# Optimization experiments

Hardware: AMD Instinct MI355X
Metric: run time of the kernel (lower is better)

Reference implementation:

```python
import jax, jax.numpy as jnp
import numpy as np

N_USERS = 20000
N_ITEMS = 20000
H0, H1, H2 = 256, 512, 256  # hidden = [256, 512, 256]
B = 4096
LN_EPS = 1e-5


def _ln(x, g, b):
    m = jnp.mean(x, axis=-1, keepdims=True)
    v = jnp.mean(jnp.square(x - m), axis=-1, keepdims=True)
    return (x - m) * jax.lax.rsqrt(v + LN_EPS) * g + b


def setup_inputs() -> dict:
    key = jax.random.key(0)
    ks = jax.random.split(key, 12)
    s = 0.02
    inp = {
        "user_idx": jax.random.randint(ks[0], (B,), 0, N_USERS),
        "item_idx": jax.random.randint(ks[1], (B,), 0, N_ITEMS),
        # (n_users+1, n_items+1) binary interaction matrix, stored as bool
        "interactions": jax.random.bernoulli(ks[2], 0.05, (N_USERS + 1, N_ITEMS + 1)),
        # proj_u / proj_i (bias=False), torch Linear layout (out, in)
        "Wu": jax.random.normal(ks[3], (H0, N_ITEMS), jnp.float32) * s,
        "Wi": jax.random.normal(ks[4], (H0, N_USERS), jnp.float32) * s,
        # rep_u: Linear(H0,H1)+LN+ReLU, Linear(H1,H2)+LN+ReLU (dropout=eval identity)
        "W1": jax.random.normal(ks[5], (H1, H0), jnp.float32) * s,
        "b1": jnp.zeros((H1,), jnp.float32),
        "g1": jnp.ones((H1,), jnp.float32),
        "be1": jnp.zeros((H1,), jnp.float32),
        "W2": jax.random.normal(ks[6], (H2, H1), jnp.float32) * s,
        "b2": jnp.zeros((H2,), jnp.float32),
        "g2": jnp.ones((H2,), jnp.float32),
        "be2": jnp.zeros((H2,), jnp.float32),
        # logit layer
        "Wl": jax.random.normal(ks[7], (1, H2), jnp.float32) * s,
        "bl": jnp.zeros((1,), jnp.float32),
    }
    return inp


def reference(user_idx, item_idx, interactions, Wu, Wi, W1, b1, g1, be1,
              W2, b2, g2, be2, Wl, bl):
    b_arange = jnp.arange(user_idx.shape[0])

    # --- user history embedding: gather row, zero target item, project, MLP ---
    u_slice = interactions[user_idx, :-1].astype(jnp.float32)      # (B, n_items)
    u_slice = u_slice.at[b_arange, item_idx].set(0.0)
    u = u_slice @ Wu.T                                             # (B, H0)
    u = jax.nn.relu(_ln(u @ W1.T + b1, g1, be1))                   # (B, H1)
    user_rep = jax.nn.relu(_ln(u @ W2.T + b2, g2, be2))            # (B, H2)

    # --- item history embedding: gather column, zero target user, project ---
    i_slice = interactions.T[item_idx][:, :-1].astype(jnp.float32)  # (B, n_users)
    i_slice = i_slice.at[b_arange, user_idx].set(0.0)
    item_rep = i_slice @ Wi.T                                      # (B, H0); rep_i is an empty Sequential in source

    pred_vector = user_rep * item_rep                              # (B, H2) == (B, H0)
    logit = (pred_vector @ Wl.T + bl).squeeze(-1)                  # (B,)
    return logit
```

## Files before the change

### kernel.cpp

```cpp
#include <hip/hip_runtime.h>

#define N_USERS 20000
#define N_ITEMS 20000
#define NI1     20001
#define HB      4096
#define H0      256
#define H1      512
#define H2      256
#define PKW     632
#define PKB     (PKW*4)
#define NWF     12501251

typedef unsigned short u16;
typedef unsigned char  u8;
typedef unsigned int   u32;
typedef unsigned long long u64;

typedef __attribute__((ext_vector_type(8))) __bf16 bf16x8;
typedef __attribute__((ext_vector_type(4))) float  f32x4;

__device__ __forceinline__ u16 f2bf(float f) {
  u32 u = __float_as_uint(f);
  u32 r = (u + 0x7FFFu + ((u >> 16) & 1u)) >> 16;
  return (u16)r;
}

__global__ __launch_bounds__(256) void k_detect(const u8* __restrict__ inter,
                                                int* __restrict__ flag) {
  __shared__ u32 cnt[4];
  if (threadIdx.x < 4) cnt[threadIdx.x] = 0;
  __syncthreads();
  u32 loc0 = 0, loc1 = 0, loc2 = 0, loc3 = 0;
  for (int i = threadIdx.x; i < 16384; i += 256) {
    u32 w = ((const u32*)inter)[i];
    loc0 += (w & 0x000000FFu) ? 1u : 0u;
    loc1 += (w & 0x0000FF00u) ? 1u : 0u;
    loc2 += (w & 0x00FF0000u) ? 1u : 0u;
    loc3 += (w & 0xFF000000u) ? 1u : 0u;
  }
  atomicAdd(&cnt[0], loc0); atomicAdd(&cnt[1], loc1);
  atomicAdd(&cnt[2], loc2); atomicAdd(&cnt[3], loc3);
  __syncthreads();
  if (threadIdx.x == 0) {
    int lay;
    if (cnt[1] != 0)      lay = 0;
    else if (cnt[0] != 0) lay = 1;
    else                  lay = 2;
    *flag = lay;
  }
}

__global__ __launch_bounds__(256) void k_packF(const u8* __restrict__ inter,
                                               u32* __restrict__ pkF,
                                               const int* __restrict__ flag) {
  int lay = *flag;
  __shared__ u32 nibs[4][8][64];
  const size_t TE = (size_t)NI1 * NI1;
  const int NG = (int)((TE + 8191) / 8192);
  int wave = threadIdx.x >> 6, lane = threadIdx.x & 63;
  const u32* base32 = (const u32*)inter;
  for (int g = blockIdx.x; g < NG; g += gridDim.x) {
    size_t E0 = (size_t)g * 8192 + (size_t)wave * 2048;
    bool full = ((size_t)(g + 1) * 8192) <= TE;
    if (lay != 0) {
      if (full) {
        #pragma unroll
        for (int t = 0; t < 8; ++t) {
          size_t e = E0 + (size_t)t * 256 + lane * 4;
          uint4 v = *(const uint4*)(base32 + e);
          nibs[wave][t][lane] = (v.x ? 1u : 0u) | (v.y ? 2u : 0u) |
                                (v.z ? 4u : 0u) | (v.w ? 8u : 0u);
        }
      } else {
        #pragma unroll
        for (int t = 0; t < 8; ++t) {
          size_t e = E0 + (size_t)t * 256 + lane * 4;
          u32 n = 0;
          #pragma unroll
          for (int c = 0; c < 4; ++c)
            if (e + c < TE && base32[e + c]) n |= 1u << c;
          nibs[wave][t][lane] = n;
        }
      }
    } else {
      #pragma unroll
      for (int t = 0; t < 8; ++t) {
        size_t e = E0 + (size_t)t * 256 + lane * 4;
        u32 n = 0;
        #pragma unroll
        for (int c = 0; c < 4; ++c)
          if (e + c < TE && inter[e + c]) n |= 1u << c;
        nibs[wave][t][lane] = n;
      }
    }
    __syncthreads();
    {
      int t = lane >> 3, j = lane & 7;
      u32 wrd = 0;
      #pragma unroll
      for (int k = 0; k < 8; ++k) wrd |= nibs[wave][t][8 * j + k] << (4 * k);
      size_t wg = (size_t)g * 256 + wave * 64 + lane;
      if (wg < NWF) pkF[wg] = wrd;
    }
    __syncthreads();
  }
}

__global__ __launch_bounds__(256) void k_realign(const u32* __restrict__ pkF,
                                                 u32* __restrict__ pk) {
  int r = blockIdx.x;
  int base = 625 * r + (r >> 5);
  int s = r & 31;
  for (int w = threadIdx.x; w < PKW; w += 256) {
    u32 val = 0;
    if (w < 625) {
      u32 lo = pkF[base + w];
      u32 hi = pkF[base + w + 1];
      val = s ? ((lo >> s) | (hi << (32 - s))) : lo;
    }
    pk[(size_t)r * PKW + w] = val;
  }
}

#define HDSTEP(J, M)                                      \
  _Pragma("unroll")                                       \
  for (int k = 0; k < 32; ++k) if (!(k & J)) {            \
    u32 tt = (a[k] ^ (a[k | J] >> J)) & M;                \
    a[k] ^= tt; a[k | J] ^= tt << J;                      \
  }

__global__ __launch_bounds__(256) void k_bitT(const u32* __restrict__ pk,
                                              u32* __restrict__ pkT) {
  __shared__ u32 in_l[512][17];
  __shared__ u32 out_l[32][16][17];
  int t = threadIdx.x;
  int vt = blockIdx.x % 40, wt = blockIdx.x / 40;
  int v0 = vt * 16, wc0 = wt * 16;
  int lw = t & 15, lr = t >> 4;
  for (int ch = 0; ch < 32; ++ch) {
    int rloc = ch * 16 + lr;
    int R = v0 * 32 + rloc;
    int W = wc0 + lw;
    u32 val = 0;
    if (R < N_USERS && W < PKW) val = pk[(size_t)R * PKW + W];
    in_l[rloc][lw] = val;
  }
  __syncthreads();
  u32 a[32];
  #pragma unroll
  for (int j = 0; j < 32; ++j) a[j] = in_l[lr * 32 + j][lw];
  HDSTEP(16, 0x0000FFFFu)
  HDSTEP(8,  0x00FF00FFu)
  HDSTEP(4,  0x0F0F0F0Fu)
  HDSTEP(2,  0x33333333u)
  HDSTEP(1,  0x55555555u)
  #pragma unroll
  for (int i = 0; i < 32; ++i) out_l[i][lw][lr] = __brev(a[31 - i]);
  __syncthreads();
  for (int ch = 0; ch < 32; ++ch) {
    int rloc = ch * 16 + lr;
    int C = wc0 * 32 + rloc;
    int V = v0 + lw;
    if (C < N_ITEMS && V < PKW)
      pkT[(size_t)C * PKW + V] = out_l[rloc & 31][rloc >> 5][lw];
  }
}

__global__ __launch_bounds__(256) void k_convert2(const float* __restrict__ Wu,
                                                  const float* __restrict__ Wi,
                                                  u16* __restrict__ Wub,
                                                  u16* __restrict__ Wib) {
  const int n4 = H0 * N_ITEMS / 4;
  int stride = gridDim.x * 256;
  for (int i = blockIdx.x * 256 + threadIdx.x; i < 2 * n4; i += stride) {
    const float* in = (i < n4) ? Wu : Wi;
    u16* out = (i < n4) ? Wub : Wib;
    int idx = (i < n4) ? i : i - n4;
    float4 v = ((const float4*)in)[idx];
    u64 p = (u64)f2bf(v.x) | ((u64)f2bf(v.y) << 16) |
            ((u64)f2bf(v.z) << 32) | ((u64)f2bf(v.w) << 48);
    ((u64*)out)[idx] = p;
  }
}

__global__ __launch_bounds__(256) void k_transpose2(const float* __restrict__ W1,
                                                    float* __restrict__ W1T,
                                                    const float* __restrict__ W2,
                                                    float* __restrict__ W2T) {
  __shared__ float tile[32][33];
  int bid = blockIdx.x;
  const float* in; float* out; int R, C, b;
  if (bid < 128) { in = W1; out = W1T; R = H1; C = H0; b = bid; }
  else           { in = W2; out = W2T; R = H2; C = H1; b = bid - 128; }
  int nbx = C >> 5;
  int bx = b % nbx, by = b / nbx;
  int c0 = bx * 32, r0 = by * 32;
  int lx = threadIdx.x & 31, ly = threadIdx.x >> 5;
  #pragma unroll
  for (int j = 0; j < 4; ++j)
    tile[ly + 8*j][lx] = in[(size_t)(r0 + ly + 8*j) * C + c0 + lx];
  __syncthreads();
  #pragma unroll
  for (int j = 0; j < 4; ++j)
    out[(size_t)(c0 + ly + 8*j) * R + r0 + lx] = tile[lx][ly + 8*j];
}

__global__ __launch_bounds__(1024) void k_sort(const int* __restrict__ item_idx,
                                               int* __restrict__ perm) {
  __shared__ u32 cnt[N_ITEMS];
  __shared__ u32 tsum[1024];
  int t = threadIdx.x;
  for (int i = t; i < N_ITEMS; i += 1024) cnt[i] = 0;
  __syncthreads();
  for (int b = t; b < HB; b += 1024) atomicAdd(&cnt[item_idx[b]], 1u);
  __syncthreads();
  u32 s = 0;
  int base = t * 20;
  for (int j = 0; j < 20; ++j) { int i = base + j; if (i < N_ITEMS) s += cnt[i]; }
  tsum[t] = s;
  __syncthreads();
  for (int off = 1; off < 1024; off <<= 1) {
    u32 v = (t >= off) ? tsum[t - off] : 0u;
    __syncthreads();
    tsum[t] += v;
    __syncthreads();
  }
  u32 run = tsum[t] - s;
  for (int j = 0; j < 20; ++j) {
    int i = base + j;
    if (i < N_ITEMS) { u32 c = cnt[i]; cnt[i] = run; run += c; }
  }
  __syncthreads();
  for (int b = t; b < HB; b += 1024) {
    int v = item_idx[b];
    u32 pos = atomicAdd(&cnt[v], 1u);
    perm[pos] = b;
  }
}

__global__ __launch_bounds__(256, 4) void k_gemm(
    const u32* __restrict__ pk, const u32* __restrict__ pkT,
    const int* __restrict__ user_idx, const int* __restrict__ item_idx,
    const int* __restrict__ perm,
    const u16* __restrict__ Wub, const u16* __restrict__ Wib,
    float* __restrict__ u0, float* __restrict__ u0b,
    float* __restrict__ ir, float* __restrict__ irb) {
  __shared__ __attribute__((aligned(16))) u16 Bls[2][32 * 256];
  __shared__ __attribute__((aligned(16))) uint2 lut8[16];
  __shared__ u32 pbase[128];
  __shared__ int prow[128];

  int bid = blockIdx.x;
  int kh = bid >> 9;
  int mode_item = (bid >> 8) & 1;
  int lid = bid & 255;
  int M0 = (lid >> 3) * 128;
  int N0 = (lid & 7) * 32;
  int tid = threadIdx.x;
  const u16* Wb = mode_item ? Wib : Wub;
  const u8* Pk = (const u8*)(mode_item ? pkT : pk);
  float* Cout = mode_item ? (kh ? irb : ir) : (kh ? u0b : u0);

  if (tid < 16) {
    u32 v = tid;
    lut8[tid].x = ((v & 1u) ? 0x3F80u : 0u) | ((v & 2u) ? 0x3F800000u : 0u);
    lut8[tid].y = ((v & 4u) ? 0x3F80u : 0u) | ((v & 8u) ? 0x3F800000u : 0u);
  }
  if (tid < 128) {
    int s = M0 + tid;
    if (mode_item) { int p = perm[s]; prow[tid] = p; pbase[tid] = (u32)item_idx[p] * PKB; }
    else           { prow[tid] = s;   pbase[tid] = (u32)user_idx[s] * PKB; }
  }
  __syncthreads();

  f32x4 acc[2][2];
  #pragma unroll
  for (int a = 0; a < 2; ++a)
    #pragma unroll
    for (int b = 0; b < 2; ++b)
      #pragma unroll
      for (int j = 0; j < 4; ++j) acc[a][b][j] = 0.f;

  int lane = tid & 63, wave = tid >> 6;
  int WM = wave * 32;
  int lrow = lane & 15;
  int lk8 = lane >> 4;
  int sh = lk8 * 8;

  u32 pb0 = pbase[WM + lrow];
  u32 pb1 = pbase[WM + 16 + lrow];

  int bsn[4], bsk[4], bso[4];
  #pragma unroll
  for (int i = 0; i < 4; ++i) {
    int id = tid + 256 * i;
    int n = id >> 5, c8 = id & 31;
    bsn[i] = N0 + n;
    bsk[i] = c8 * 8;
    bso[i] = n * 256 + ((c8 * 8) ^ ((n & 7) << 3));
  }

  int k0_beg = kh ? 10240 : 0;
  int k0_end = kh ? 20224 : 10240;

  uint4 breg[4];
  #pragma unroll
  for (int i = 0; i < 4; ++i) {
    int k = k0_beg + bsk[i];
    breg[i] = make_uint4(0u, 0u, 0u, 0u);
    if (k < N_ITEMS) breg[i] = *(const uint4*)&Wb[(size_t)bsn[i] * N_ITEMS + k];
  }
  #pragma unroll
  for (int i = 0; i < 4; ++i) *(uint4*)&Bls[0][bso[i]] = breg[i];
  int bc0 = k0_beg >> 3;
  uint4 ca0l = *(const uint4*)(Pk + pb0 + bc0);
  uint4 ca0h = *(const uint4*)(Pk + pb0 + bc0 + 16);
  uint4 ca1l = *(const uint4*)(Pk + pb1 + bc0);
  uint4 ca1h = *(const uint4*)(Pk + pb1 + bc0 + 16);
  __syncthreads();

  int cur = 0;
  for (int k0 = k0_beg; k0 < k0_end; k0 += 256) {
    int k1 = k0 + 256;
    bool more = k1 < k0_end;
    uint4 na0l, na0h, na1l, na1h;
    if (more) {
      #pragma unroll
      for (int i = 0; i < 4; ++i) {
        int k = k1 + bsk[i];
        breg[i] = make_uint4(0u, 0u, 0u, 0u);
        if (k < N_ITEMS) breg[i] = *(const uint4*)&Wb[(size_t)bsn[i] * N_ITEMS + k];
      }
      int nbc = k1 >> 3;
      na0l = *(const uint4*)(Pk + pb0 + nbc);
      na0h = *(const uint4*)(Pk + pb0 + nbc + 16);
      na1l = *(const uint4*)(Pk + pb1 + nbc);
      na1h = *(const uint4*)(Pk + pb1 + nbc + 16);
    }
    u32 qw0[8] = {ca0l.x, ca0l.y, ca0l.z, ca0l.w, ca0h.x, ca0h.y, ca0h.z, ca0h.w};
    u32 qw1[8] = {ca1l.x, ca1l.y, ca1l.z, ca1l.w, ca1h.x, ca1h.y, ca1h.z, ca1h.w};
    #pragma unroll
    for (int kki = 0; kki < 8; ++kki) {
      u32 b0 = (qw0[kki] >> sh) & 0xFFu;
      u32 b1 = (qw1[kki] >> sh) & 0xFFu;
      union { u32 w[4]; bf16x8 v; } a0, a1;
      uint2 l0 = lut8[b0 & 15u], h0 = lut8[b0 >> 4];
      uint2 l1 = lut8[b1 & 15u], h1 = lut8[b1 >> 4];
      a0.w[0] = l0.x; a0.w[1] = l0.y; a0.w[2] = h0.x; a0.w[3] = h0.y;
      a1.w[0] = l1.x; a1.w[1] = l1.y; a1.w[2] = h1.x; a1.w[3] = h1.y;
      bf16x8 bfr[2];
      #pragma unroll
      for (int fn = 0; fn < 2; ++fn) {
        int n = fn * 16 + lrow;
        bfr[fn] = *(const bf16x8*)&Bls[cur][n * 256 + ((kki * 32 + sh) ^ ((n & 7) << 3))];
      }
      acc[0][0] = __builtin_amdgcn_mfma_f32_16x16x32_bf16(a0.v, bfr[0], acc[0][0], 0, 0, 0);
      acc[0][1] = __builtin_amdgcn_mfma_f32_16x16x32_bf16(a0.v, bfr[1], acc[0][1], 0, 0, 0);
      acc[1][0] = __builtin_amdgcn_mfma_f32_16x16x32_bf16(a1.v, bfr[0], acc[1][0], 0, 0, 0);
      acc[1][1] = __builtin_amdgcn_mfma_f32_16x16x32_bf16(a1.v, bfr[1], acc[1][1], 0, 0, 0);
    }
    if (more) {
      #pragma unroll
      for (int i = 0; i < 4; ++i) *(uint4*)&Bls[cur ^ 1][bso[i]] = breg[i];
      ca0l = na0l; ca0h = na0h; ca1l = na1l; ca1h = na1h;
    }
    __syncthreads();
    cur ^= 1;
  }

  int crow0 = (lane >> 4) * 4;
  int ccol = lane & 15;
  #pragma unroll
  for (int fm = 0; fm < 2; ++fm)
    #pragma unroll
    for (int fn = 0; fn < 2; ++fn) {
      f32x4 v = acc[fm][fn];
      int col = N0 + fn * 16 + ccol;
      #pragma unroll
      for (int j = 0; j < 4; ++j) {
        int rl = WM + fm * 16 + crow0 + j;
        Cout[(size_t)prow[rl] * H0 + col] = v[j];
      }
    }
}

__global__ __launch_bounds__(256) void k_mlp(
    const u32* __restrict__ pk,
    const int* __restrict__ user_idx, const int* __restrict__ item_idx,
    const float* __restrict__ Wu, const float* __restrict__ Wi,
    const float* __restrict__ u0, const float* __restrict__ u0b,
    const float* __restrict__ ir, const float* __restrict__ irb,
    const float* __restrict__ W1T, const float* __restrict__ b1,
    const float* __restrict__ g1, const float* __restrict__ be1,
    const float* __restrict__ W2T, const float* __restrict__ b2,
    const float* __restrict__ g2, const float* __restrict__ be2,
    const float* __restrict__ Wl, const float* __restrict__ bl,
    float* __restrict__ out) {
  __shared__ __attribute__((aligned(16))) float xl[16][H0];
  __shared__ __attribute__((aligned(16))) float h1l[16][H1];
  __shared__ int flagL[16], uL[16], iL[16];

  int tid = threadIdx.x, lane = tid & 63, wave = tid >> 6;
  int b0 = blockIdx.x * 16;

  if (tid < 16) {
    int b = b0 + tid;
    int uu = user_idx[b], ii = item_idx[b];
    uL[tid] = uu; iL[tid] = ii;
    u8 byte = ((const u8*)pk)[(size_t)uu * PKB + (ii >> 3)];
    flagL[tid] = (byte >> (ii & 7)) & 1;
  }
  __syncthreads();

  for (int idx = tid; idx < 16 * H0; idx += 256) {
    int rr = idx >> 8, h = idx & 255;
    size_t o = (size_t)(b0 + rr) * H0 + h;
    float x = u0[o] + u0b[o];
    if (flagL[rr]) x -= Wu[(size_t)h * N_ITEMS + iL[rr]];
    xl[rr][h] = x;
  }
  __syncthreads();

  float a0[16], a1[16];
  #pragma unroll
  for (int rr = 0; rr < 16; ++rr) { a0[rr] = 0.f; a1[rr] = 0.f; }
  for (int k4 = 0; k4 < H0 / 4; ++k4) {
    int k = k4 * 4;
    float w0a = W1T[(size_t)(k+0)*H1 + tid], w0b = W1T[(size_t)(k+0)*H1 + tid + 256];
    float w1a = W1T[(size_t)(k+1)*H1 + tid], w1b = W1T[(size_t)(k+1)*H1 + tid + 256];
    float w2a = W1T[(size_t)(k+2)*H1 + tid], w2b = W1T[(size_t)(k+2)*H1 + tid + 256];
    float w3a = W1T[(size_t)(k+3)*H1 + tid], w3b = W1T[(size_t)(k+3)*H1 + tid + 256];
    #pragma unroll
    for (int rr = 0; rr < 16; ++rr) {
      float4 x = *(const float4*)&xl[rr][k];
      a0[rr] += x.x * w0a + x.y * w1a + x.z * w2a + x.w * w3a;
      a1[rr] += x.x * w0b + x.y * w1b + x.z * w2b + x.w * w3b;
    }
  }
  #pragma unroll
  for (int rr = 0; rr < 16; ++rr) {
    h1l[rr][tid]       = a0[rr] + b1[tid];
    h1l[rr][tid + 256] = a1[rr] + b1[tid + 256];
  }
  __syncthreads();

  for (int rr = wave; rr < 16; rr += 4) {
    float s = 0.f;
    #pragma unroll
    for (int j = 0; j < 8; ++j) s += h1l[rr][lane + 64 * j];
    #pragma unroll
    for (int off = 32; off; off >>= 1) s += __shfl_xor(s, off);
    float m = s * (1.f / H1);
    float v = 0.f;
    #pragma unroll
    for (int j = 0; j < 8; ++j) { float d = h1l[rr][lane + 64*j] - m; v += d * d; }
    #pragma unroll
    for (int off = 32; off; off >>= 1) v += __shfl_xor(v, off);
    float inv = rsqrtf(v * (1.f / H1) + 1e-5f);
    #pragma unroll
    for (int j = 0; j < 8; ++j) {
      int o = lane + 64 * j;
      float y = (h1l[rr][o] - m) * inv * g1[o] + be1[o];
      h1l[rr][o] = fmaxf(y, 0.f);
    }
  }
  __syncthreads();

  float a2[16];
  #pragma unroll
  for (int rr = 0; rr < 16; ++rr) a2[rr] = 0.f;
  for (int k4 = 0; k4 < H1 / 4; ++k4) {
    int k = k4 * 4;
    float w0 = W2T[(size_t)(k+0)*H2 + tid];
    float w1 = W2T[(size_t)(k+1)*H2 + tid];
    float w2 = W2T[(size_t)(k+2)*H2 + tid];
    float w3 = W2T[(size_t)(k+3)*H2 + tid];
    #pragma unroll
    for (int rr = 0; rr < 16; ++rr) {
      float4 x = *(const float4*)&h1l[rr][k];
      a2[rr] += x.x * w0 + x.y * w1 + x.z * w2 + x.w * w3;
    }
  }
  __syncthreads();
  #pragma unroll
  for (int rr = 0; rr < 16; ++rr) xl[rr][tid] = a2[rr] + b2[tid];
  __syncthreads();

  for (int rr = wave; rr < 16; rr += 4) {
    float s = 0.f;
    #pragma unroll
    for (int j = 0; j < 4; ++j) s += xl[rr][lane + 64 * j];
    #pragma unroll
    for (int off = 32; off; off >>= 1) s += __shfl_xor(s, off);
    float m = s * (1.f / H2);
    float v = 0.f;
    #pragma unroll
    for (int j = 0; j < 4; ++j) { float d = xl[rr][lane + 64*j] - m; v += d * d; }
    #pragma unroll
    for (int off = 32; off; off >>= 1) v += __shfl_xor(v, off);
    float inv = rsqrtf(v * (1.f / H2) + 1e-5f);
    #pragma unroll
    for (int j = 0; j < 4; ++j) {
      int o = lane + 64 * j;
      float y = (xl[rr][o] - m) * inv * g2[o] + be2[o];
      xl[rr][o] = fmaxf(y, 0.f);
    }
  }
  __syncthreads();

  for (int rr = wave; rr < 16; rr += 4) {
    int b = b0 + rr;
    int flg = flagL[rr], uu = uL[rr];
    float s = 0.f;
    #pragma unroll
    for (int j = 0; j < 4; ++j) {
      int h = lane + 64 * j;
      size_t o = (size_t)b * H0 + h;
      float irv = ir[o] + irb[o];
      if (flg) irv -= Wi[(size_t)h * N_USERS + uu];
      s += xl[rr][h] * irv * Wl[h];
    }
    #pragma unroll
    for (int off = 32; off; off >>= 1) s += __shfl_xor(s, off);
    if (lane == 0) out[b] = s + bl[0];
  }
}

extern "C" void kernel_launch(void* const* d_in, const int* in_sizes, int n_in,
                              void* d_out, int out_size, void* d_ws, size_t ws_size,
                              hipStream_t stream) {
  const int*   user_idx = (const int*)d_in[0];
  const int*   item_idx = (const int*)d_in[1];
  const u8*    inter    = (const u8*)d_in[2];
  const float* Wu  = (const float*)d_in[3];
  const float* Wi  = (const float*)d_in[4];
  const float* W1  = (const float*)d_in[5];
  const float* b1  = (const float*)d_in[6];
  const float* g1  = (const float*)d_in[7];
  const float* be1 = (const float*)d_in[8];
  const float* W2  = (const float*)d_in[9];
  const float* b2  = (const float*)d_in[10];
  const float* g2  = (const float*)d_in[11];
  const float* be2 = (const float*)d_in[12];
  const float* Wl  = (const float*)d_in[13];
  const float* bl  = (const float*)d_in[14];
  float* out = (float*)d_out;

  char* ws = (char*)d_ws;
  size_t off = 0;
  auto alloc = [&](size_t bytes) {
    size_t o = off;
    off = (off + bytes + 255) & ~(size_t)255;
    return o;
  };
  int*   flag = (int*)  (ws + alloc(4));
  u32*   pkF  = (u32*)  (ws + alloc((size_t)(NWF + 64) * 4));
  u32*   pk   = (u32*)  (ws + alloc((size_t)N_USERS * PKB));
  u32*   pkT  = (u32*)  (ws + alloc((size_t)N_ITEMS * PKB));
  u16*   Wub  = (u16*)  (ws + alloc((size_t)H0 * N_ITEMS * 2));
  u16*   Wib  = (u16*)  (ws + alloc((size_t)H0 * N_USERS * 2));
  float* W1T  = (float*)(ws + alloc((size_t)H0 * H1 * 4));
  float* W2T  = (float*)(ws + alloc((size_t)H1 * H2 * 4));
  float* u0   = (float*)(ws + alloc((size_t)HB * H0 * 4));
  float* u0b  = (float*)(ws + alloc((size_t)HB * H0 * 4));
  float* ir   = (float*)(ws + alloc((size_t)HB * H0 * 4));
  float* irb  = (float*)(ws + alloc((size_t)HB * H0 * 4));
  int*   perm = (int*)  (ws + alloc((size_t)HB * 4));

  k_detect<<<1, 256, 0, stream>>>(inter, flag);
  k_packF<<<3072, 256, 0, stream>>>(inter, pkF, flag);
  k_realign<<<N_USERS, 256, 0, stream>>>(pkF, pk);
  k_bitT<<<1600, 256, 0, stream>>>(pk, pkT);
  k_convert2<<<1024, 256, 0, stream>>>(Wu, Wi, Wub, Wib);
  k_transpose2<<<256, 256, 0, stream>>>(W1, W1T, W2, W2T);
  k_sort<<<1, 1024, 0, stream>>>(item_idx, perm);
  k_gemm<<<1024, 256, 0, stream>>>(pk, pkT, user_idx, item_idx, perm, Wub, Wib,
                                   u0, u0b, ir, irb);
  k_mlp<<<256, 256, 0, stream>>>(pk, user_idx, item_idx, Wu, Wi, u0, u0b, ir, irb,
                                 W1T, b1, g1, be1, W2T, b2, g2, be2, Wl, bl, out);
}
```

Measured before the change: 657.3 us.

## Load GEMM weight tiles directly to LDS from zero-padded bf16 weights

Converts Wu/Wi to bf16 with rows padded to a multiple of 256 and zero-filled, so the GEMM no longer needs bounds checks on the K tail. The B-operand tile loads now use global_load_lds to write straight into shared memory with a pre-swizzled source address, instead of staging through registers and storing after compute. This frees VGPRs and removes the separate LDS store phase. k_bitT also shares one LDS buffer between its input and output staging, adding a barrier, to cut shared-memory use. The risks are that the direct-to-LDS layout must match the existing swizzle exactly, and the padded weights use slightly more workspace.

```diff
diff --git a/kernel.cpp b/kernel.cpp
--- a/kernel.cpp
+++ b/kernel.cpp
@@ -10,6 +10,7 @@
 #define PKW     632
 #define PKB     (PKW*4)
 #define NWF     12501251
+#define PADN    20224
 
 typedef unsigned short u16;
 typedef unsigned char  u8;
@@ -23,6 +24,12 @@
   u32 u = __float_as_uint(f);
   u32 r = (u + 0x7FFFu + ((u >> 16) & 1u)) >> 16;
   return (u16)r;
+}
+
+__device__ __forceinline__ void gload16(const u16* gp, u16* lp) {
+  __builtin_amdgcn_global_load_lds(
+      (const __attribute__((address_space(1))) u32*)gp,
+      (__attribute__((address_space(3))) u32*)lp, 16, 0, 0);
 }
 
 __global__ __launch_bounds__(256) void k_detect(const u8* __restrict__ inter,
@@ -131,8 +138,7 @@
 
 __global__ __launch_bounds__(256) void k_bitT(const u32* __restrict__ pk,
                                               u32* __restrict__ pkT) {
-  __shared__ u32 in_l[512][17];
-  __shared__ u32 out_l[32][16][17];
+  __shared__ u32 buf[512 * 17];
   int t = threadIdx.x;
   int vt = blockIdx.x % 40, wt = blockIdx.x / 40;
   int v0 = vt * 16, wc0 = wt * 16;
@@ -143,43 +149,55 @@
     int W = wc0 + lw;
     u32 val = 0;
     if (R < N_USERS && W < PKW) val = pk[(size_t)R * PKW + W];
-    in_l[rloc][lw] = val;
+    buf[rloc * 17 + lw] = val;
   }
   __syncthreads();
   u32 a[32];
   #pragma unroll
-  for (int j = 0; j < 32; ++j) a[j] = in_l[lr * 32 + j][lw];
+  for (int j = 0; j < 32; ++j) a[j] = buf[(lr * 32 + j) * 17 + lw];
   HDSTEP(16, 0x0000FFFFu)
   HDSTEP(8,  0x00FF00FFu)
   HDSTEP(4,  0x0F0F0F0Fu)
   HDSTEP(2,  0x33333333u)
   HDSTEP(1,  0x55555555u)
-  #pragma unroll
-  for (int i = 0; i < 32; ++i) out_l[i][lw][lr] = __brev(a[31 - i]);
+  __syncthreads();
+  #pragma unroll
+  for (int i = 0; i < 32; ++i) buf[(i * 16 + lw) * 17 + lr] = __brev(a[31 - i]);
   __syncthreads();
   for (int ch = 0; ch < 32; ++ch) {
     int rloc = ch * 16 + lr;
     int C = wc0 * 32 + rloc;
     int V = v0 + lw;
     if (C < N_ITEMS && V < PKW)
-      pkT[(size_t)C * PKW + V] = out_l[rloc & 31][rloc >> 5][lw];
-  }
-}
-
-__global__ __launch_bounds__(256) void k_convert2(const float* __restrict__ Wu,
-                                                  const float* __restrict__ Wi,
-                                                  u16* __restrict__ Wub,
-                                                  u16* __restrict__ Wib) {
-  const int n4 = H0 * N_ITEMS / 4;
-  int stride = gridDim.x * 256;
-  for (int i = blockIdx.x * 256 + threadIdx.x; i < 2 * n4; i += stride) {
-    const float* in = (i < n4) ? Wu : Wi;
-    u16* out = (i < n4) ? Wub : Wib;
-    int idx = (i < n4) ? i : i - n4;
-    float4 v = ((const float4*)in)[idx];
-    u64 p = (u64)f2bf(v.x) | ((u64)f2bf(v.y) << 16) |
-            ((u64)f2bf(v.z) << 32) | ((u64)f2bf(v.w) << 48);
-    ((u64*)out)[idx] = p;
+      pkT[(size_t)C * PKW + V] = buf[((rloc & 31) * 16 + (rloc >> 5)) * 17 + lw];
+  }
+}
+
+__global__ __launch_bounds__(256) void k_convert2p(const float* __restrict__ Wu,
+                                                   const float* __restrict__ Wi,
+                                                   u16* __restrict__ Wub,
+                                                   u16* __restrict__ Wib) {
+  int r = blockIdx.x;
+  const float* src = (r < 256) ? Wu : Wi;
+  u16* dst = (r < 256) ? Wub : Wib;
+  int rr = r & 255;
+  src += (size_t)rr * N_ITEMS;
+  dst += (size_t)rr * PADN;
+  for (int k8 = threadIdx.x * 8; k8 < PADN; k8 += 256 * 8) {
+    u64 p = 0;
+    if (k8 < N_ITEMS) {
+      float4 v0 = *(const float4*)(src + k8);
+      float4 v1 = *(const float4*)(src + k8 + 4);
+      p = (u64)f2bf(v0.x) | ((u64)f2bf(v0.y) << 16) |
+          ((u64)f2bf(v0.z) << 32) | ((u64)f2bf(v0.w) << 48);
+      u64 q = (u64)f2bf(v1.x) | ((u64)f2bf(v1.y) << 16) |
+              ((u64)f2bf(v1.z) << 32) | ((u64)f2bf(v1.w) << 48);
+      ((u64*)(dst + k8))[0] = p;
+      ((u64*)(dst + k8))[1] = q;
+    } else {
+      ((u64*)(dst + k8))[0] = 0;
+      ((u64*)(dst + k8))[1] = 0;
+    }
   }
 }
 
@@ -290,28 +308,21 @@
   u32 pb0 = pbase[WM + lrow];
   u32 pb1 = pbase[WM + 16 + lrow];
 
-  int bsn[4], bsk[4], bso[4];
+  const u16* gsrc[4];
+  int ldso[4];
   #pragma unroll
   for (int i = 0; i < 4; ++i) {
     int id = tid + 256 * i;
     int n = id >> 5, c8 = id & 31;
-    bsn[i] = N0 + n;
-    bsk[i] = c8 * 8;
-    bso[i] = n * 256 + ((c8 * 8) ^ ((n & 7) << 3));
+    gsrc[i] = Wb + (size_t)(N0 + n) * PADN + (c8 ^ (n & 7)) * 8;
+    ldso[i] = (wave * 64 + 256 * i) * 8;
   }
 
   int k0_beg = kh ? 10240 : 0;
   int k0_end = kh ? 20224 : 10240;
 
-  uint4 breg[4];
-  #pragma unroll
-  for (int i = 0; i < 4; ++i) {
-    int k = k0_beg + bsk[i];
-    breg[i] = make_uint4(0u, 0u, 0u, 0u);
-    if (k < N_ITEMS) breg[i] = *(const uint4*)&Wb[(size_t)bsn[i] * N_ITEMS + k];
-  }
-  #pragma unroll
-  for (int i = 0; i < 4; ++i) *(uint4*)&Bls[0][bso[i]] = breg[i];
+  #pragma unroll
+  for (int i = 0; i < 4; ++i) gload16(gsrc[i] + k0_beg, &Bls[0][ldso[i]]);
   int bc0 = k0_beg >> 3;
   uint4 ca0l = *(const uint4*)(Pk + pb0 + bc0);
   uint4 ca0h = *(const uint4*)(Pk + pb0 + bc0 + 16);
@@ -326,11 +337,7 @@
     uint4 na0l, na0h, na1l, na1h;
     if (more) {
       #pragma unroll
-      for (int i = 0; i < 4; ++i) {
-        int k = k1 + bsk[i];
-        breg[i] = make_uint4(0u, 0u, 0u, 0u);
-        if (k < N_ITEMS) breg[i] = *(const uint4*)&Wb[(size_t)bsn[i] * N_ITEMS + k];
-      }
+      for (int i = 0; i < 4; ++i) gload16(gsrc[i] + k1, &Bls[cur ^ 1][ldso[i]]);
       int nbc = k1 >> 3;
       na0l = *(const uint4*)(Pk + pb0 + nbc);
       na0h = *(const uint4*)(Pk + pb0 + nbc + 16);
@@ -359,11 +366,7 @@
       acc[1][0] = __builtin_amdgcn_mfma_f32_16x16x32_bf16(a1.v, bfr[0], acc[1][0], 0, 0, 0);
       acc[1][1] = __builtin_amdgcn_mfma_f32_16x16x32_bf16(a1.v, bfr[1], acc[1][1], 0, 0, 0);
     }
-    if (more) {
-      #pragma unroll
-      for (int i = 0; i < 4; ++i) *(uint4*)&Bls[cur ^ 1][bso[i]] = breg[i];
-      ca0l = na0l; ca0h = na0h; ca1l = na1l; ca1h = na1h;
-    }
+    if (more) { ca0l = na0l; ca0h = na0h; ca1l = na1l; ca1h = na1h; }
     __syncthreads();
     cur ^= 1;
   }
@@ -557,8 +560,8 @@
   u32*   pkF  = (u32*)  (ws + alloc((size_t)(NWF + 64) * 4));
   u32*   pk   = (u32*)  (ws + alloc((size_t)N_USERS * PKB));
   u32*   pkT  = (u32*)  (ws + alloc((size_t)N_ITEMS * PKB));
-  u16*   Wub  = (u16*)  (ws + alloc((size_t)H0 * N_ITEMS * 2));
-  u16*   Wib  = (u16*)  (ws + alloc((size_t)H0 * N_USERS * 2));
+  u16*   Wub  = (u16*)  (ws + alloc((size_t)H0 * PADN * 2));
+  u16*   Wib  = (u16*)  (ws + alloc((size_t)H0 * PADN * 2));
   float* W1T  = (float*)(ws + alloc((size_t)H0 * H1 * 4));
   float* W2T  = (float*)(ws + alloc((size_t)H1 * H2 * 4));
   float* u0   = (float*)(ws + alloc((size_t)HB * H0 * 4));
@@ -571,7 +574,7 @@
   k_packF<<<3072, 256, 0, stream>>>(inter, pkF, flag);
   k_realign<<<N_USERS, 256, 0, stream>>>(pkF, pk);
   k_bitT<<<1600, 256, 0, stream>>>(pk, pkT);
-  k_convert2<<<1024, 256, 0, stream>>>(Wu, Wi, Wub, Wib);
+  k_convert2p<<<512, 256, 0, stream>>>(Wu, Wi, Wub, Wib);
   k_transpose2<<<256, 256, 0, stream>>>(W1, W1T, W2, W2T);
   k_sort<<<1, 1024, 0, stream>>>(item_idx, perm);
   k_gemm<<<1024, 256, 0, stream>>>(pk, pkT, user_idx, item_idx, perm, Wub, Wib,
```

Result: faster. 630.0 us (-4.2%).
